# Optimization experiments

Hardware: AMD Instinct MI355X
Metric: run time of the kernel (lower is better)

## Reference

```python
import jax, jax.numpy as jnp
import numpy as np


def _axial_mha(x, Wq, Wk, Wv, Wo, bo, n_head, axis):
    # x: (B, T, H, W, C) channels-last video features
    B, T, H, W, C = x.shape
    d = C // n_head
    scale = 1.0 / np.sqrt(d)

    def proj(w):
        return (x @ w.T).reshape(B, T, H, W, n_head, d)

    q, k, v = proj(Wq), proj(Wk), proj(Wv)
    if axis == 'w':  # attend along width
        s = jnp.einsum('bthwnd,bthvnd->bthnwv', q, k) * scale
        a = jax.nn.softmax(s, axis=-1)
        o = jnp.einsum('bthnwv,bthvnd->bthwnd', a, v)
    elif axis == 'h':  # attend along height
        s = jnp.einsum('bthwnd,btgwnd->btwnhg', q, k) * scale
        a = jax.nn.softmax(s, axis=-1)
        o = jnp.einsum('btwnhg,btgwnd->bthwnd', a, v)
    else:  # 't' attend along time
        s = jnp.einsum('bthwnd,bshwnd->bhwnts', q, k) * scale
        a = jax.nn.softmax(s, axis=-1)
        o = jnp.einsum('bhwnts,bshwnd->bthwnd', a, v)
    o = o.reshape(B, T, H, W, C)
    return o @ Wo.T + bo


def setup_inputs() -> dict:
    key = jax.random.key(0)
    ks = jax.random.split(key, 16)
    B, C, T, H, W = 4, 512, 16, 32, 32
    std = 1.0 / np.sqrt(C)
    inp = {'x': jax.random.normal(ks[0], (B, C, T, H, W), jnp.float32)}
    i = 1
    for ax in ('w', 'h', 't'):
        for nm in ('wq', 'wk', 'wv', 'wo'):
            inp[f'{nm}_{ax}'] = jax.random.normal(ks[i], (C, C), jnp.float32) * std
            i += 1
        inp[f'bo_{ax}'] = jnp.zeros((C,), jnp.float32)
    inp['n_head'] = 8
    return inp


def reference(x, wq_w, wk_w, wv_w, wo_w, bo_w,
              wq_h, wk_h, wv_h, wo_h, bo_h,
              wq_t, wk_t, wv_t, wo_t, bo_t, n_head):
    xt = jnp.moveaxis(x, 1, -1)  # (B, T, H, W, C)
    out = (_axial_mha(xt, wq_w, wk_w, wv_w, wo_w, bo_w, n_head, 'w')
           + _axial_mha(xt, wq_h, wk_h, wv_h, wo_h, bo_h, n_head, 'h')
           + _axial_mha(xt, wq_t, wk_t, wv_t, wo_t, bo_t, n_head, 't'))
    return jnp.moveaxis(out, -1, 1)  # (B, C, T, H, W)
```

## Files before the change

kernel.cpp:

```cpp
#include <hip/hip_runtime.h>

typedef float f4 __attribute__((ext_vector_type(4)));
typedef int i4 __attribute__((ext_vector_type(4)));
typedef __bf16 bf16x8 __attribute__((ext_vector_type(8)));
typedef unsigned short u16;

#define DEV static __device__ __forceinline__

DEV f4 mfma_bf16(bf16x8 a, bf16x8 b, f4 c) {
  return __builtin_amdgcn_mfma_f32_16x16x32_bf16(a, b, c, 0, 0, 0);
}

DEV bf16x8 ld_frag(const u16* p) {
  union { i4 i; bf16x8 b; } u;
  u.i = *(const i4*)p;
  return u.b;
}

DEV u16 f2bf(float f) {
  union { float f; unsigned int u; } v; v.f = f;
  return (u16)((v.u + 0x7fffu + ((v.u >> 16) & 1u)) >> 16);
}

DEV void async_cp16(const void* g, void* l) {
  __builtin_amdgcn_global_load_lds((const __attribute__((address_space(1))) void*)g,
                                   (__attribute__((address_space(3))) void*)l, 16, 0, 0);
}

__global__ __launch_bounds__(256) void k_transpose_x(const float* __restrict__ x,
                                                     u16* __restrict__ xt) {
  __shared__ float tile[32][33];
  const int b = blockIdx.z;
  const int thw0 = blockIdx.x * 32;
  const int c0 = blockIdx.y * 32;
  const int tc = threadIdx.x & 31;
  const int tr = threadIdx.x >> 5;
#pragma unroll
  for (int i = 0; i < 4; i++) {
    int c = tr + i * 8;
    tile[c][tc] = x[(long)(b * 512 + c0 + c) * 16384 + thw0 + tc];
  }
  __syncthreads();
#pragma unroll
  for (int i = 0; i < 4; i++) {
    int r = tr + i * 8;
    xt[(long)(b * 16384 + thw0 + r) * 512 + c0 + tc] = f2bf(tile[tc][r]);
  }
}

__global__ __launch_bounds__(256) void k_prep_w(
    const float* wq_w, const float* wk_w, const float* wv_w, const float* wo_w, const float* bo_w,
    const float* wq_h, const float* wk_h, const float* wv_h, const float* wo_h, const float* bo_h,
    const float* wq_t, const float* wk_t, const float* wv_t, const float* wo_t, const float* bo_t,
    u16* Wqkv, u16* WoCat, float* bo) {
  const int idx = blockIdx.x * 256 + threadIdx.x;
  if (idx < 2359296) {
    int j = idx >> 9, ci = idx & 511;
    int sel = j >> 9, co = j & 511;
    const float* s;
    switch (sel) {
      case 0: s = wq_w; break; case 1: s = wk_w; break; case 2: s = wv_w; break;
      case 3: s = wq_h; break; case 4: s = wk_h; break; case 5: s = wv_h; break;
      case 6: s = wq_t; break; case 7: s = wk_t; break; default: s = wv_t; break;
    }
    Wqkv[idx] = f2bf(s[co * 512 + ci]);
  } else if (idx < 2359296 + 786432) {
    int t = idx - 2359296;
    int c = t / 1536, j2 = t - c * 1536;
    int a = j2 >> 9, ci = j2 & 511;
    const float* s = (a == 0) ? wo_w : (a == 1) ? wo_h : wo_t;
    WoCat[t] = f2bf(s[c * 512 + ci]);
  } else if (idx < 2359296 + 786432 + 512) {
    int c = idx - (2359296 + 786432);
    bo[c] = bo_w[c] + bo_h[c] + bo_t[c];
  }
}

template <int NK, int EPI, int NT, int MT, bool MMINOR>
__global__ __launch_bounds__(512, 2) void k_gemm256(
    const u16* __restrict__ A, const u16* __restrict__ Bt,
    void* __restrict__ Co, const float* __restrict__ bias, int ldc) {
  constexpr int K = NK * 32;
  __shared__ __attribute__((aligned(16))) u16 lds[65536];
  u16* ldsA = lds;
  u16* ldsB = lds + 32768;

  const int tid = threadIdx.x;
  const int lane = tid & 63, wave = tid >> 6;
  const int cl = lane & 15, q = lane >> 4;
  const int wr = wave >> 2, wc = wave & 3;

  const int bid = blockIdx.x;
  const int orig = (bid & 7) * ((NT * MT) >> 3) + (bid >> 3);
  const int my = MMINOR ? (orig % MT) : (orig / NT);
  const int nx = MMINOR ? (orig / MT) : (orig % NT);
  const long m0 = (long)my * 256;
  const long n0 = (long)nx * 256;
  const u16* Ab = A + m0 * K;
  const u16* Bb = Bt + n0 * K;

  long g_off[2];
  int dslot[2];
#pragma unroll
  for (int i = 0; i < 2; i++) {
    int s = i * 512 + tid;
    int row = s >> 2;
    int g = ((s & 3) - (row >> 2)) & 3;
    g_off[i] = (long)row * K + g * 8;
    dslot[i] = (i * 512 + (tid & 448)) * 8;
  }

  f4 acc[8][4];
  {
    f4 z; z[0] = z[1] = z[2] = z[3] = 0.f;
#pragma unroll
    for (int m = 0; m < 8; m++)
#pragma unroll
      for (int n = 0; n < 4; n++) acc[m][n] = z;
  }

#pragma unroll
  for (int t = 0; t < 3; t++) {
#pragma unroll
    for (int i = 0; i < 2; i++) {
      async_cp16(Ab + g_off[i] + t * 32, ldsA + t * 8192 + dslot[i]);
      async_cp16(Bb + g_off[i] + t * 32, ldsB + t * 8192 + dslot[i]);
    }
  }
  asm volatile("s_waitcnt vmcnt(8)\n\ts_barrier" ::: "memory");

  const int ch = ((q + (cl >> 2)) & 3) * 8;
  const int rowA = (wr * 128 + cl) * 32 + ch;
  const int rowB = (wc * 64 + cl) * 32 + ch;

  const u16* pa0 = Ab + g_off[0] + 96;
  const u16* pa1 = Ab + g_off[1] + 96;
  const u16* pb0 = Bb + g_off[0] + 96;
  const u16* pb1 = Bb + g_off[1] + 96;

#define STAGE(sb)                                              \
  {                                                            \
    async_cp16(pa0, ldsA + (sb) * 8192 + dslot[0]);            \
    async_cp16(pb0, ldsB + (sb) * 8192 + dslot[0]);            \
    async_cp16(pa1, ldsA + (sb) * 8192 + dslot[1]);            \
    async_cp16(pb1, ldsB + (sb) * 8192 + dslot[1]);            \
    pa0 += 32; pa1 += 32; pb0 += 32; pb1 += 32;                \
  }

#define COMPUTE(buf)                                           \
  {                                                            \
    const u16* bA = ldsA + (buf) * 8192;                       \
    const u16* bB = ldsB + (buf) * 8192;                       \
    bf16x8 af[8], bfr[4];                                      \
    _Pragma("unroll")                                          \
    for (int m = 0; m < 8; m++) af[m] = ld_frag(bA + rowA + m * 512);  \
    _Pragma("unroll")                                          \
    for (int n = 0; n < 4; n++) bfr[n] = ld_frag(bB + rowB + n * 512); \
    __builtin_amdgcn_s_setprio(1);                             \
    _Pragma("unroll")                                          \
    for (int m = 0; m < 8; m++)                                \
      _Pragma("unroll")                                        \
      for (int n = 0; n < 4; n++)                              \
        acc[m][n] = mfma_bf16(af[m], bfr[n], acc[m][n]);       \
    __builtin_amdgcn_s_setprio(0);                             \
  }

  for (int tt = 0; tt < NK - 4; tt += 4) {
#pragma unroll
    for (int u = 0; u < 4; u++) {
      STAGE((u + 3) & 3);
      COMPUTE(u);
      asm volatile("s_waitcnt vmcnt(8)\n\ts_barrier" ::: "memory");
    }
  }
  STAGE(3);
  COMPUTE(0);
  asm volatile("s_waitcnt vmcnt(8)\n\ts_barrier" ::: "memory");
  COMPUTE(1);
  asm volatile("s_waitcnt vmcnt(4)\n\ts_barrier" ::: "memory");
  COMPUTE(2);
  asm volatile("s_waitcnt vmcnt(0)\n\ts_barrier" ::: "memory");
  COMPUTE(3);
#undef STAGE
#undef COMPUTE

  if (EPI == 0) {
    __syncthreads();
    u16* myl = lds + wave * 4608;
    u16* CoB = (u16*)Co;
#pragma unroll
    for (int h = 0; h < 2; h++) {
      if (h) __syncthreads();
#pragma unroll
      for (int m = 0; m < 4; m++)
#pragma unroll
        for (int n = 0; n < 4; n++)
#pragma unroll
          for (int r = 0; r < 4; r++)
            myl[(m * 16 + q * 4 + r) * 72 + n * 16 + cl] = f2bf(acc[h * 4 + m][n][r]);
#pragma unroll
      for (int it = 0; it < 8; it++) {
        int lr = it * 8 + (lane >> 3);
        int lc = (lane & 7) * 8;
        i4 v = *(const i4*)(myl + lr * 72 + lc);
        *(i4*)(CoB + (m0 + wr * 128 + h * 64 + lr) * ldc + n0 + wc * 64 + lc) = v;
      }
    }
  } else {
    float* Cf = (float*)Co;
#pragma unroll
    for (int m = 0; m < 8; m++)
#pragma unroll
      for (int r = 0; r < 4; r++) {
        int c = (int)m0 + wr * 128 + m * 16 + q * 4 + r;
        float bv = bias[c];
#pragma unroll
        for (int n = 0; n < 4; n++) {
          long nn = n0 + wc * 64 + n * 16 + cl;
          long b = nn >> 14, thw = nn & 16383;
          Cf[((b * 512 + c) << 14) + thw] = acc[m][n][r] + bv;
        }
      }
  }
}

template <int L>
__global__ __launch_bounds__(64) void k_attn(
    const u16* __restrict__ QKV, u16* __restrict__ Oc,
    int inner, int istride, int ostride, int obase, int tstride) {
  constexpr int NT = L / 16;
  __shared__ __attribute__((aligned(16))) u16 sQ[2048];
  __shared__ __attribute__((aligned(16))) u16 sK[2048];
  __shared__ __attribute__((aligned(16))) u16 sVt[2560];
  __shared__ __attribute__((aligned(16))) u16 sPbuf[(L == 16) ? 1280 : 1];
  u16* sP = (L == 16) ? sPbuf : sQ;
  const int lane = threadIdx.x;
  const int cl = lane & 15, q = lane >> 4;
  const int g = blockIdx.x, head = blockIdx.y;
  const long tok0 = (long)(g / inner) * ostride + (long)(g % inner) * istride;
  const long rs = (long)tstride * 1536;
  const u16* qb = QKV + tok0 * 1536 + head * 64;
  const u16* kb = qb + 512;
  const u16* vb = qb + 1024;

  if (L == 16) {
    unsigned int* z1 = (unsigned int*)sVt;
    for (int i = lane; i < 1280; i += 64) z1[i] = 0;
    unsigned int* z2 = (unsigned int*)sPbuf;
    for (int i = lane; i < 640; i += 64) z2[i] = 0;
  }

#pragma unroll
  for (int i = 0; i < L / 8; i++) {
    int s = i * 64 + lane;
    int row = s >> 3;
    int gc = (s & 7) ^ (row & 7);
    async_cp16(qb + row * rs + gc * 8, (char*)sQ + i * 1024);
    async_cp16(kb + row * rs + gc * 8, (char*)sK + i * 1024);
  }
#pragma unroll
  for (int i = 0; i < L / 8; i++) {
    int s = i * 64 + lane;
    int row = s >> 3, c8 = s & 7;
    union { i4 v; u16 h[8]; } raw;
    raw.v = *(const i4*)(vb + row * rs + c8 * 8);
#pragma unroll
    for (int j = 0; j < 8; j++) sVt[(c8 * 8 + j) * 40 + row] = raw.h[j];
  }
  __syncthreads();

  f4 sacc[NT][NT];
  { f4 z; z[0]=z[1]=z[2]=z[3]=0.f;
    for (int a = 0; a < NT; a++) for (int b2 = 0; b2 < NT; b2++) sacc[a][b2] = z; }
#pragma unroll
  for (int kk = 0; kk < 2; kk++) {
    bf16x8 qf[NT], kf[NT];
#pragma unroll
    for (int t = 0; t < NT; t++) {
      int row = t * 16 + cl;
      int ch = (kk * 4 + q) ^ (row & 7);
      qf[t] = ld_frag(sQ + row * 64 + ch * 8);
      kf[t] = ld_frag(sK + row * 64 + ch * 8);
    }
#pragma unroll
    for (int rt = 0; rt < NT; rt++)
#pragma unroll
      for (int ct = 0; ct < NT; ct++)
        sacc[rt][ct] = mfma_bf16(qf[rt], kf[ct], sacc[rt][ct]);
  }

#pragma unroll
  for (int rt = 0; rt < NT; rt++)
#pragma unroll
    for (int ct = 0; ct < NT; ct++)
#pragma unroll
      for (int i = 0; i < 4; i++) sacc[rt][ct][i] *= 0.125f;
#pragma unroll
  for (int rt = 0; rt < NT; rt++)
#pragma unroll
    for (int i = 0; i < 4; i++) {
      float m = sacc[rt][0][i];
#pragma unroll
      for (int ct = 1; ct < NT; ct++) m = fmaxf(m, sacc[rt][ct][i]);
      for (int off = 1; off < 16; off <<= 1) m = fmaxf(m, __shfl_xor(m, off, 64));
      float ssum = 0.f;
#pragma unroll
      for (int ct = 0; ct < NT; ct++) {
        float p = __expf(sacc[rt][ct][i] - m);
        sacc[rt][ct][i] = p;
        ssum += p;
      }
      for (int off = 1; off < 16; off <<= 1) ssum += __shfl_xor(ssum, off, 64);
      float inv = 1.0f / ssum;
#pragma unroll
      for (int ct = 0; ct < NT; ct++) sacc[rt][ct][i] *= inv;
    }

#pragma unroll
  for (int rt = 0; rt < NT; rt++)
#pragma unroll
    for (int ct = 0; ct < NT; ct++)
#pragma unroll
      for (int i = 0; i < 4; i++)
        sP[(rt * 16 + q * 4 + i) * 40 + ct * 16 + cl] = f2bf(sacc[rt][ct][i]);
  __syncthreads();

  bf16x8 pf[NT], vf[4];
#pragma unroll
  for (int mt = 0; mt < NT; mt++) pf[mt] = ld_frag(sP + (mt * 16 + cl) * 40 + q * 8);
#pragma unroll
  for (int nt = 0; nt < 4; nt++) vf[nt] = ld_frag(sVt + (nt * 16 + cl) * 40 + q * 8);
  f4 oacc[NT][4];
  { f4 z; z[0]=z[1]=z[2]=z[3]=0.f;
    for (int a = 0; a < NT; a++) for (int b2 = 0; b2 < 4; b2++) oacc[a][b2] = z; }
#pragma unroll
  for (int mt = 0; mt < NT; mt++)
#pragma unroll
    for (int nt = 0; nt < 4; nt++)
      oacc[mt][nt] = mfma_bf16(pf[mt], vf[nt], oacc[mt][nt]);

#pragma unroll
  for (int mt = 0; mt < NT; mt++)
#pragma unroll
    for (int i = 0; i < 4; i++) {
      int r = mt * 16 + q * 4 + i;
      u16* dst = Oc + (tok0 + (long)r * tstride) * 1536 + obase + head * 64;
#pragma unroll
      for (int nt = 0; nt < 4; nt++) dst[nt * 16 + cl] = f2bf(oacc[mt][nt][i]);
    }
}

extern "C" void kernel_launch(void* const* d_in, const int* in_sizes, int n_in,
                              void* d_out, int out_size, void* d_ws, size_t ws_size,
                              hipStream_t stream) {
  (void)in_sizes; (void)n_in; (void)out_size; (void)ws_size;
  const float* x    = (const float*)d_in[0];
  const float* wq_w = (const float*)d_in[1];
  const float* wk_w = (const float*)d_in[2];
  const float* wv_w = (const float*)d_in[3];
  const float* wo_w = (const float*)d_in[4];
  const float* bo_w = (const float*)d_in[5];
  const float* wq_h = (const float*)d_in[6];
  const float* wk_h = (const float*)d_in[7];
  const float* wv_h = (const float*)d_in[8];
  const float* wo_h = (const float*)d_in[9];
  const float* bo_h = (const float*)d_in[10];
  const float* wq_t = (const float*)d_in[11];
  const float* wk_t = (const float*)d_in[12];
  const float* wv_t = (const float*)d_in[13];
  const float* wo_t = (const float*)d_in[14];
  const float* bo_t = (const float*)d_in[15];

  char* ws = (char*)d_ws;
  u16* xt    = (u16*)(ws);
  u16* qkv   = (u16*)(ws + 67108864L);
  u16* oc    = (u16*)(ws + 268435456L);
  u16* Wqkv  = (u16*)(ws + 469762048L);
  u16* WoCat = (u16*)(ws + 474480640L);
  float* bo  = (float*)(ws + 476053504L);

  k_transpose_x<<<dim3(512, 16, 4), 256, 0, stream>>>(x, xt);
  k_prep_w<<<dim3(12290), 256, 0, stream>>>(wq_w, wk_w, wv_w, wo_w, bo_w,
                                            wq_h, wk_h, wv_h, wo_h, bo_h,
                                            wq_t, wk_t, wv_t, wo_t, bo_t,
                                            Wqkv, WoCat, bo);
  for (int a = 0; a < 3; a++) {
    k_gemm256<16, 0, 6, 256, false><<<dim3(1536), 512, 0, stream>>>(
        xt, Wqkv + (long)a * 1536 * 512, qkv, nullptr, 1536);
    if (a == 0)
      k_attn<32><<<dim3(2048, 8), 64, 0, stream>>>(qkv, oc, 1, 0, 32, 0, 1);
    else if (a == 1)
      k_attn<32><<<dim3(2048, 8), 64, 0, stream>>>(qkv, oc, 32, 1, 1024, 512, 32);
    else
      k_attn<16><<<dim3(4096, 8), 64, 0, stream>>>(qkv, oc, 1024, 1, 16384, 1024, 1024);
  }
  k_gemm256<48, 1, 256, 2, true><<<dim3(512), 512, 0, stream>>>(
      WoCat, oc, (float*)d_out, bo, 0);
}
```

Before: 961.8 us.

## Restructure GEMM main loop to 64-wide K tiles with double-buffered quarter-staged prefetch

Rewrites the k_gemm256 main loop so each LDS stage holds a 64-wide K slice, using an XOR swizzle, instead of four 32-wide buffers. Each slice is split into A/B halves that are prefetched in quarters between groups of MFMAs. Barriers are placed so loads, LDS fragment reads and MFMA groups interleave in a ping-pong schedule, aiming to hide global-load latency and cut LDS bank conflicts. The cost is many more barriers per tile and a fragile hand-built schedule, and the NK template arguments at the call sites are halved to match.

```diff
diff --git a/kernel.cpp b/kernel.cpp
--- a/kernel.cpp
+++ b/kernel.cpp
@@ -80,10 +80,9 @@
 __global__ __launch_bounds__(512, 2) void k_gemm256(
     const u16* __restrict__ A, const u16* __restrict__ Bt,
     void* __restrict__ Co, const float* __restrict__ bias, int ldc) {
-  constexpr int K = NK * 32;
+  constexpr int K = NK * 64;
+  constexpr int NIT = NK / 2;
   __shared__ __attribute__((aligned(16))) u16 lds[65536];
-  u16* ldsA = lds;
-  u16* ldsB = lds + 32768;
 
   const int tid = threadIdx.x;
   const int lane = tid & 63, wave = tid >> 6;
@@ -99,16 +98,68 @@
   const u16* Ab = A + m0 * K;
   const u16* Bb = Bt + n0 * K;
 
-  long g_off[2];
-  int dslot[2];
+  long goff[2];
+  int sdst[2];
 #pragma unroll
   for (int i = 0; i < 2; i++) {
     int s = i * 512 + tid;
-    int row = s >> 2;
-    int g = ((s & 3) - (row >> 2)) & 3;
-    g_off[i] = (long)row * K + g * 8;
-    dslot[i] = (i * 512 + (tid & 448)) * 8;
-  }
+    int row = s >> 3;
+    int c = (s & 7) ^ (row & 7);
+    goff[i] = (long)row * K + c * 8;
+    sdst[i] = (i * 512 + (tid & 448)) * 8;
+  }
+
+#define STG(op, h, t)                                                        \
+  {                                                                          \
+    const u16* gb_ = (op) ? Bb : Ab;                                         \
+    u16* lb_ = lds + ((t) & 1) * 32768 + (op) * 16384 + (h) * 8192;          \
+    _Pragma("unroll")                                                        \
+    for (int i_ = 0; i_ < 2; i_++)                                           \
+      async_cp16(gb_ + goff[i_] + (long)(h) * 128 * K + (t) * 64,            \
+                 lb_ + sdst[i_]);                                            \
+  }
+#define BAR() __builtin_amdgcn_s_barrier()
+#define WAITV(N) asm volatile("s_waitcnt vmcnt(" #N ")" ::: "memory")
+
+  const int pk0 = (q ^ (cl & 7)) * 8;
+  const int pk1 = ((q + 4) ^ (cl & 7)) * 8;
+  const int arow = (wr * 128 + cl) * 64;
+  const int brow = (wc * 64 + cl) * 64;
+
+  bf16x8 a[4][2], bl[2][2], bh[2][2];
+
+#define LD_A(bb, mh)                                                         \
+  _Pragma("unroll")                                                          \
+  for (int m_ = 0; m_ < 4; m_++) {                                           \
+    const u16* p_ = lds + (bb) * 32768 + arow + (mh) * 4096 + m_ * 1024;     \
+    a[m_][0] = ld_frag(p_ + pk0);                                            \
+    a[m_][1] = ld_frag(p_ + pk1);                                            \
+  }
+#define LD_BL(bb)                                                            \
+  _Pragma("unroll")                                                          \
+  for (int n_ = 0; n_ < 2; n_++) {                                           \
+    const u16* p_ = lds + (bb) * 32768 + 16384 + brow + n_ * 1024;           \
+    bl[n_][0] = ld_frag(p_ + pk0);                                           \
+    bl[n_][1] = ld_frag(p_ + pk1);                                           \
+  }
+#define LD_BH(bb)                                                            \
+  _Pragma("unroll")                                                          \
+  for (int n_ = 0; n_ < 2; n_++) {                                           \
+    const u16* p_ = lds + (bb) * 32768 + 16384 + brow + 2048 + n_ * 1024;    \
+    bh[n_][0] = ld_frag(p_ + pk0);                                           \
+    bh[n_][1] = ld_frag(p_ + pk1);                                           \
+  }
+#define MM(mh, nh, B)                                                        \
+  __builtin_amdgcn_s_setprio(1);                                             \
+  _Pragma("unroll")                                                          \
+  for (int m_ = 0; m_ < 4; m_++)                                             \
+    _Pragma("unroll")                                                        \
+    for (int n_ = 0; n_ < 2; n_++)                                           \
+      _Pragma("unroll")                                                      \
+      for (int ks_ = 0; ks_ < 2; ks_++)                                      \
+        acc[(mh) * 4 + m_][(nh) * 2 + n_] =                                  \
+            mfma_bf16(a[m_][ks_], B[n_][ks_], acc[(mh) * 4 + m_][(nh) * 2 + n_]); \
+  __builtin_amdgcn_s_setprio(0);
 
   f4 acc[8][4];
   {
@@ -119,70 +170,48 @@
       for (int n = 0; n < 4; n++) acc[m][n] = z;
   }
 
-#pragma unroll
-  for (int t = 0; t < 3; t++) {
-#pragma unroll
-    for (int i = 0; i < 2; i++) {
-      async_cp16(Ab + g_off[i] + t * 32, ldsA + t * 8192 + dslot[i]);
-      async_cp16(Bb + g_off[i] + t * 32, ldsB + t * 8192 + dslot[i]);
-    }
-  }
-  asm volatile("s_waitcnt vmcnt(8)\n\ts_barrier" ::: "memory");
-
-  const int ch = ((q + (cl >> 2)) & 3) * 8;
-  const int rowA = (wr * 128 + cl) * 32 + ch;
-  const int rowB = (wc * 64 + cl) * 32 + ch;
-
-  const u16* pa0 = Ab + g_off[0] + 96;
-  const u16* pa1 = Ab + g_off[1] + 96;
-  const u16* pb0 = Bb + g_off[0] + 96;
-  const u16* pb1 = Bb + g_off[1] + 96;
-
-#define STAGE(sb)                                              \
-  {                                                            \
-    async_cp16(pa0, ldsA + (sb) * 8192 + dslot[0]);            \
-    async_cp16(pb0, ldsB + (sb) * 8192 + dslot[0]);            \
-    async_cp16(pa1, ldsA + (sb) * 8192 + dslot[1]);            \
-    async_cp16(pb1, ldsB + (sb) * 8192 + dslot[1]);            \
-    pa0 += 32; pa1 += 32; pb0 += 32; pb1 += 32;                \
-  }
-
-#define COMPUTE(buf)                                           \
-  {                                                            \
-    const u16* bA = ldsA + (buf) * 8192;                       \
-    const u16* bB = ldsB + (buf) * 8192;                       \
-    bf16x8 af[8], bfr[4];                                      \
-    _Pragma("unroll")                                          \
-    for (int m = 0; m < 8; m++) af[m] = ld_frag(bA + rowA + m * 512);  \
-    _Pragma("unroll")                                          \
-    for (int n = 0; n < 4; n++) bfr[n] = ld_frag(bB + rowB + n * 512); \
-    __builtin_amdgcn_s_setprio(1);                             \
-    _Pragma("unroll")                                          \
-    for (int m = 0; m < 8; m++)                                \
-      _Pragma("unroll")                                        \
-      for (int n = 0; n < 4; n++)                              \
-        acc[m][n] = mfma_bf16(af[m], bfr[n], acc[m][n]);       \
-    __builtin_amdgcn_s_setprio(0);                             \
-  }
-
-  for (int tt = 0; tt < NK - 4; tt += 4) {
-#pragma unroll
-    for (int u = 0; u < 4; u++) {
-      STAGE((u + 3) & 3);
-      COMPUTE(u);
-      asm volatile("s_waitcnt vmcnt(8)\n\ts_barrier" ::: "memory");
-    }
-  }
-  STAGE(3);
-  COMPUTE(0);
-  asm volatile("s_waitcnt vmcnt(8)\n\ts_barrier" ::: "memory");
-  COMPUTE(1);
-  asm volatile("s_waitcnt vmcnt(4)\n\ts_barrier" ::: "memory");
-  COMPUTE(2);
-  asm volatile("s_waitcnt vmcnt(0)\n\ts_barrier" ::: "memory");
-  COMPUTE(3);
-#undef STAGE
-#undef COMPUTE
+  STG(1, 0, 0); STG(1, 1, 0); STG(0, 0, 0); STG(0, 1, 0);
+  STG(1, 0, 1); STG(1, 1, 1);
+  WAITV(4);
+  BAR();
+
+#define ITER_BODY(t, MORE)                                                   \
+                                           \
+  LD_A(0, 0); LD_BL(0); STG(0, 0, (t) + 1);                                  \
+  BAR(); MM(0, 0, bl); BAR();                                                \
+  LD_BH(0); STG(0, 1, (t) + 1);                                              \
+  BAR(); MM(0, 1, bh); BAR();                                                \
+  LD_A(0, 1); if (MORE) STG(1, 0, (t) + 2);                                  \
+  BAR(); MM(1, 0, bl); BAR();                                                \
+  if (MORE) { STG(1, 1, (t) + 2); WAITV(4); } else { WAITV(0); }             \
+  BAR(); MM(1, 1, bh); BAR();                                                \
+                                         \
+  LD_A(1, 0); LD_BL(1); if (MORE) STG(0, 0, (t) + 2);                        \
+  BAR(); MM(0, 0, bl); BAR();                                                \
+  LD_BH(1); if (MORE) STG(0, 1, (t) + 2);                                    \
+  BAR(); MM(0, 1, bh); BAR();                                                \
+  LD_A(1, 1); if (MORE) STG(1, 0, (t) + 3);                                  \
+  BAR(); MM(1, 0, bl); BAR();                                                \
+  if (MORE) { STG(1, 1, (t) + 3); WAITV(4); } else { WAITV(0); }             \
+  BAR(); MM(1, 1, bh); BAR();
+
+#pragma unroll 1
+  for (int it = 0; it < NIT - 1; ++it) {
+    const int t = 2 * it;
+    ITER_BODY(t, true)
+  }
+  {
+    const int t = 2 * (NIT - 1);
+    ITER_BODY(t, false)
+  }
+#undef ITER_BODY
+#undef MM
+#undef LD_A
+#undef LD_BL
+#undef LD_BH
+#undef STG
+#undef WAITV
+#undef BAR
 
   if (EPI == 0) {
     __syncthreads();
@@ -385,7 +414,7 @@
                                             wq_t, wk_t, wv_t, wo_t, bo_t,
                                             Wqkv, WoCat, bo);
   for (int a = 0; a < 3; a++) {
-    k_gemm256<16, 0, 6, 256, false><<<dim3(1536), 512, 0, stream>>>(
+    k_gemm256<8, 0, 6, 256, false><<<dim3(1536), 512, 0, stream>>>(
         xt, Wqkv + (long)a * 1536 * 512, qkv, nullptr, 1536);
     if (a == 0)
       k_attn<32><<<dim3(2048, 8), 64, 0, stream>>>(qkv, oc, 1, 0, 32, 0, 1);
@@ -394,6 +423,6 @@
     else
       k_attn<16><<<dim3(4096, 8), 64, 0, stream>>>(qkv, oc, 1024, 1, 16384, 1024, 1024);
   }
-  k_gemm256<48, 1, 256, 2, true><<<dim3(512), 512, 0, stream>>>(
+  k_gemm256<24, 1, 256, 2, true><<<dim3(512), 512, 0, stream>>>(
       WoCat, oc, (float*)d_out, bo, 0);
 }
```

After: 918.2 us. -4.5%, faster.

## Shrink GEMM tile to 256x128 with double-buffered LDS and higher occupancy

Applied to the files above, without the earlier changes.

Rewrites the GEMM kernel to use a 256x128 output tile per block (8 waves in a 4x2 grid, each computing 64x64) instead of 256x256. The LDS pipeline drops from a 4-stage to a 2-stage double buffer, and the shared allocation shrinks so launch bounds can target 4 blocks per CU. The LDS swizzle changes to an XOR pattern, and the grids double to 3072 and 1024 blocks. The aim is more occupancy and better wave scheduling across CUs, at the cost of less operand reuse per block and a shallower prefetch pipeline.

```diff
diff --git a/kernel.cpp b/kernel.cpp
--- a/kernel.cpp
+++ b/kernel.cpp
@@ -77,142 +77,118 @@
 }
 
 template <int NK, int EPI, int NT, int MT, bool MMINOR>
-__global__ __launch_bounds__(512, 2) void k_gemm256(
+__global__ __launch_bounds__(512, 4) void k_gemm(
     const u16* __restrict__ A, const u16* __restrict__ Bt,
     void* __restrict__ Co, const float* __restrict__ bias, int ldc) {
   constexpr int K = NK * 32;
-  __shared__ __attribute__((aligned(16))) u16 lds[65536];
-  u16* ldsA = lds;
-  u16* ldsB = lds + 32768;
+  __shared__ __attribute__((aligned(16))) u16 lds[36864];
 
   const int tid = threadIdx.x;
   const int lane = tid & 63, wave = tid >> 6;
   const int cl = lane & 15, q = lane >> 4;
-  const int wr = wave >> 2, wc = wave & 3;
+  const int wr = wave >> 1, wc = wave & 1;
 
   const int bid = blockIdx.x;
   const int orig = (bid & 7) * ((NT * MT) >> 3) + (bid >> 3);
   const int my = MMINOR ? (orig % MT) : (orig / NT);
   const int nx = MMINOR ? (orig / MT) : (orig % NT);
   const long m0 = (long)my * 256;
-  const long n0 = (long)nx * 256;
+  const long n0 = (long)nx * 128;
   const u16* Ab = A + m0 * K;
   const u16* Bb = Bt + n0 * K;
 
-  long g_off[2];
-  int dslot[2];
-#pragma unroll
-  for (int i = 0; i < 2; i++) {
-    int s = i * 512 + tid;
-    int row = s >> 2;
-    int g = ((s & 3) - (row >> 2)) & 3;
-    g_off[i] = (long)row * K + g * 8;
-    dslot[i] = (i * 512 + (tid & 448)) * 8;
-  }
-
-  f4 acc[8][4];
+  int goffA0, goffA1, goffB, dA0, dA1, dB;
+  {
+    int s0 = tid, r0 = s0 >> 2, c0 = (s0 & 3) ^ ((r0 >> 1) & 3);
+    goffA0 = r0 * K + c0 * 8;
+    int s1 = 512 + tid, r1 = s1 >> 2, c1 = (s1 & 3) ^ ((r1 >> 1) & 3);
+    goffA1 = r1 * K + c1 * 8;
+    goffB = goffA0;
+    dA0 = (tid & 448) * 8;
+    dA1 = (512 + (tid & 448)) * 8;
+    dB = (tid & 448) * 8;
+  }
+
+#define STG(t)                                                         \
+  {                                                                    \
+    u16* lb_ = lds + ((t) & 1) * 12288;                                \
+    async_cp16(Ab + goffA0 + (t) * 32, lb_ + dA0);                     \
+    async_cp16(Ab + goffA1 + (t) * 32, lb_ + dA1);                     \
+    async_cp16(Bb + goffB + (t) * 32, lb_ + 8192 + dB);                \
+  }
+#define BAR() __builtin_amdgcn_s_barrier()
+#define WAITV(N) asm volatile("s_waitcnt vmcnt(" #N ")" ::: "memory")
+#define WAITL() asm volatile("s_waitcnt lgkmcnt(0)" ::: "memory")
+
+  const int pOff = (q ^ ((cl >> 1) & 3)) * 8;
+  const int arow = (wr * 64 + cl) * 32 + pOff;
+  const int brow = (wc * 64 + cl) * 32 + pOff;
+
+  f4 acc[4][4];
   {
     f4 z; z[0] = z[1] = z[2] = z[3] = 0.f;
 #pragma unroll
-    for (int m = 0; m < 8; m++)
+    for (int m = 0; m < 4; m++)
 #pragma unroll
       for (int n = 0; n < 4; n++) acc[m][n] = z;
   }
 
-#pragma unroll
-  for (int t = 0; t < 3; t++) {
-#pragma unroll
-    for (int i = 0; i < 2; i++) {
-      async_cp16(Ab + g_off[i] + t * 32, ldsA + t * 8192 + dslot[i]);
-      async_cp16(Bb + g_off[i] + t * 32, ldsB + t * 8192 + dslot[i]);
-    }
-  }
-  asm volatile("s_waitcnt vmcnt(8)\n\ts_barrier" ::: "memory");
-
-  const int ch = ((q + (cl >> 2)) & 3) * 8;
-  const int rowA = (wr * 128 + cl) * 32 + ch;
-  const int rowB = (wc * 64 + cl) * 32 + ch;
-
-  const u16* pa0 = Ab + g_off[0] + 96;
-  const u16* pa1 = Ab + g_off[1] + 96;
-  const u16* pb0 = Bb + g_off[0] + 96;
-  const u16* pb1 = Bb + g_off[1] + 96;
-
-#define STAGE(sb)                                              \
-  {                                                            \
-    async_cp16(pa0, ldsA + (sb) * 8192 + dslot[0]);            \
-    async_cp16(pb0, ldsB + (sb) * 8192 + dslot[0]);            \
-    async_cp16(pa1, ldsA + (sb) * 8192 + dslot[1]);            \
-    async_cp16(pb1, ldsB + (sb) * 8192 + dslot[1]);            \
-    pa0 += 32; pa1 += 32; pb0 += 32; pb1 += 32;                \
-  }
-
-#define COMPUTE(buf)                                           \
-  {                                                            \
-    const u16* bA = ldsA + (buf) * 8192;                       \
-    const u16* bB = ldsB + (buf) * 8192;                       \
-    bf16x8 af[8], bfr[4];                                      \
-    _Pragma("unroll")                                          \
-    for (int m = 0; m < 8; m++) af[m] = ld_frag(bA + rowA + m * 512);  \
-    _Pragma("unroll")                                          \
-    for (int n = 0; n < 4; n++) bfr[n] = ld_frag(bB + rowB + n * 512); \
-    __builtin_amdgcn_s_setprio(1);                             \
-    _Pragma("unroll")                                          \
-    for (int m = 0; m < 8; m++)                                \
-      _Pragma("unroll")                                        \
-      for (int n = 0; n < 4; n++)                              \
-        acc[m][n] = mfma_bf16(af[m], bfr[n], acc[m][n]);       \
-    __builtin_amdgcn_s_setprio(0);                             \
-  }
-
-  for (int tt = 0; tt < NK - 4; tt += 4) {
-#pragma unroll
-    for (int u = 0; u < 4; u++) {
-      STAGE((u + 3) & 3);
-      COMPUTE(u);
-      asm volatile("s_waitcnt vmcnt(8)\n\ts_barrier" ::: "memory");
-    }
-  }
-  STAGE(3);
-  COMPUTE(0);
-  asm volatile("s_waitcnt vmcnt(8)\n\ts_barrier" ::: "memory");
-  COMPUTE(1);
-  asm volatile("s_waitcnt vmcnt(4)\n\ts_barrier" ::: "memory");
-  COMPUTE(2);
-  asm volatile("s_waitcnt vmcnt(0)\n\ts_barrier" ::: "memory");
-  COMPUTE(3);
-#undef STAGE
-#undef COMPUTE
+  STG(0);
+  STG(1);
+  WAITV(3);
+  BAR();
+
+#pragma unroll 1
+  for (int t = 0; t < NK; ++t) {
+    const u16* base = lds + (t & 1) * 12288;
+    bf16x8 af[4], bf[4];
+#pragma unroll
+    for (int m = 0; m < 4; m++) af[m] = ld_frag(base + arow + m * 512);
+#pragma unroll
+    for (int n = 0; n < 4; n++) bf[n] = ld_frag(base + 8192 + brow + n * 512);
+    WAITL();
+    BAR();
+    if (t + 2 < NK) STG(t + 2);
+    __builtin_amdgcn_s_setprio(1);
+#pragma unroll
+    for (int m = 0; m < 4; m++)
+#pragma unroll
+      for (int n = 0; n < 4; n++)
+        acc[m][n] = mfma_bf16(af[m], bf[n], acc[m][n]);
+    __builtin_amdgcn_s_setprio(0);
+    if (t + 2 < NK) WAITV(3);
+    else if (t + 1 < NK) WAITV(0);
+    BAR();
+  }
+#undef STG
+#undef BAR
+#undef WAITV
+#undef WAITL
 
   if (EPI == 0) {
-    __syncthreads();
     u16* myl = lds + wave * 4608;
     u16* CoB = (u16*)Co;
 #pragma unroll
-    for (int h = 0; h < 2; h++) {
-      if (h) __syncthreads();
-#pragma unroll
-      for (int m = 0; m < 4; m++)
-#pragma unroll
-        for (int n = 0; n < 4; n++)
-#pragma unroll
-          for (int r = 0; r < 4; r++)
-            myl[(m * 16 + q * 4 + r) * 72 + n * 16 + cl] = f2bf(acc[h * 4 + m][n][r]);
-#pragma unroll
-      for (int it = 0; it < 8; it++) {
-        int lr = it * 8 + (lane >> 3);
-        int lc = (lane & 7) * 8;
-        i4 v = *(const i4*)(myl + lr * 72 + lc);
-        *(i4*)(CoB + (m0 + wr * 128 + h * 64 + lr) * ldc + n0 + wc * 64 + lc) = v;
-      }
+    for (int m = 0; m < 4; m++)
+#pragma unroll
+      for (int n = 0; n < 4; n++)
+#pragma unroll
+        for (int r = 0; r < 4; r++)
+          myl[(m * 16 + q * 4 + r) * 72 + n * 16 + cl] = f2bf(acc[m][n][r]);
+#pragma unroll
+    for (int it = 0; it < 8; it++) {
+      int lr = it * 8 + (lane >> 3);
+      int lc = (lane & 7) * 8;
+      i4 v = *(const i4*)(myl + lr * 72 + lc);
+      *(i4*)(CoB + (m0 + wr * 64 + lr) * ldc + n0 + wc * 64 + lc) = v;
     }
   } else {
     float* Cf = (float*)Co;
 #pragma unroll
-    for (int m = 0; m < 8; m++)
+    for (int m = 0; m < 4; m++)
 #pragma unroll
       for (int r = 0; r < 4; r++) {
-        int c = (int)m0 + wr * 128 + m * 16 + q * 4 + r;
+        int c = (int)m0 + wr * 64 + m * 16 + q * 4 + r;
         float bv = bias[c];
 #pragma unroll
         for (int n = 0; n < 4; n++) {
@@ -385,7 +361,7 @@
                                             wq_t, wk_t, wv_t, wo_t, bo_t,
                                             Wqkv, WoCat, bo);
   for (int a = 0; a < 3; a++) {
-    k_gemm256<16, 0, 6, 256, false><<<dim3(1536), 512, 0, stream>>>(
+    k_gemm<16, 0, 12, 256, false><<<dim3(3072), 512, 0, stream>>>(
         xt, Wqkv + (long)a * 1536 * 512, qkv, nullptr, 1536);
     if (a == 0)
       k_attn<32><<<dim3(2048, 8), 64, 0, stream>>>(qkv, oc, 1, 0, 32, 0, 1);
@@ -394,6 +370,6 @@
     else
       k_attn<16><<<dim3(4096, 8), 64, 0, stream>>>(qkv, oc, 1024, 1, 16384, 1024, 1024);
   }
-  k_gemm256<48, 1, 256, 2, true><<<dim3(512), 512, 0, stream>>>(
+  k_gemm<48, 1, 512, 2, true><<<dim3(1024), 512, 0, stream>>>(
       WoCat, oc, (float*)d_out, bo, 0);
 }
```

New measurement: 951.3 us. Within noise of the previous version (-1.1%).
